# Kernel optimization log

Measured on AMD Instinct MI355X. Metric: run time of the kernel, lower is better.

Reference implementation:

```python
import jax, jax.numpy as jnp
import numpy as np

EPS = 1e-6

def rmsnorm(x, w):
    v = jnp.mean(x * x, axis=-1, keepdims=True)
    return x * jax.lax.rsqrt(v + EPS) * (1.0 + w)

def dense_glu(x, W, b):
    o = x @ W + b
    a, g = jnp.split(o, 2, axis=-1)
    return jax.nn.silu(a) * jax.nn.sigmoid(g)

def setup_inputs() -> dict:
    key = jax.random.key(0)
    ks = jax.random.split(key, 24)
    B, Nh, N, D, R = 2, 192, 256, 128, 20
    s_heavy = jax.random.normal(ks[0], (B, Nh, D), jnp.float32)
    v_all = jax.random.normal(ks[1], (B, N, 3, D), jnp.float32)
    rbf = jax.random.uniform(ks[2], (B, N, N, R), jnp.float32)
    dir_ij = jax.random.normal(ks[3], (B, N, N, 3), jnp.float32)
    mask_ij = jax.random.uniform(ks[4], (B, N, N), jnp.float32)
    is_hydrogen = jax.random.bernoulli(ks[5], 0.25, (B, N))
    p = lambda k, sh: 0.05 * jax.random.normal(k, sh, jnp.float32)
    return {
        "s_heavy": s_heavy, "v_all": v_all, "rbf": rbf, "dir_ij": dir_ij,
        "mask_ij": mask_ij, "is_hydrogen": is_hydrogen,
        "h_emb": jax.random.normal(ks[6], (D,), jnp.float32),
        "W_filter": p(ks[7], (R, 3 * D)), "b_filter": p(ks[8], (3 * D,)),
        "norm1_w": p(ks[9], (D,)),
        "W_i1": p(ks[10], (D, 2 * D)), "b_i1": p(ks[11], (2 * D,)),
        "W_i2": p(ks[12], (D, 3 * D)), "b_i2": p(ks[13], (3 * D,)),
        "norm2_w": p(ks[14], (D,)),
        "W_m1": p(ks[15], (2 * D, 2 * D)), "b_m1": p(ks[16], (2 * D,)),
        "W_m2": p(ks[17], (D, 3 * D)), "b_m2": p(ks[18], (3 * D,)),
        "W_mu": p(ks[19], (D, 2 * D)),
    }

def reference(s_heavy, v_all, rbf, dir_ij, mask_ij, is_hydrogen, h_emb,
              W_filter, b_filter, norm1_w, W_i1, b_i1, W_i2, b_i2,
              norm2_w, W_m1, b_m1, W_m2, b_m2, W_mu):
    B, N, _, D = v_all.shape
    Nh = s_heavy.shape[1]
    # hydrogen reinforcement: pad heavy-atom scalars to N_all, fill H slots with embedding
    s_pad = jnp.pad(s_heavy, ((0, 0), (0, N - Nh), (0, 0)))
    s_all = jnp.where(is_hydrogen[..., None], h_emb, s_pad)
    # --- interaction ---
    Wij = rbf @ W_filter + b_filter                                  # (B,N,N,3D)
    x = dense_glu(rmsnorm(s_all, norm1_w), W_i1, b_i1) @ W_i2 + b_i2  # (B,N,3D)
    x_inter = Wij * x[:, None, :, :] * mask_ij[..., None]            # (B,N,N,3D)
    dq, dmuR, dmumu = jnp.split(x_inter, 3, axis=-1)                 # each (B,N,N,D)
    q = s_all + dq.sum(axis=2)
    # dmu[b,i,r,d] = sum_j dmuR*dir + dmumu*mu_j (fused reductions over neighbor j)
    dmu = (jnp.einsum('bijd,bijr->bird', dmuR, dir_ij)
           + jnp.einsum('bijd,bjrd->bird', dmumu, v_all))            # (B,N,3,D)
    mu = v_all + dmu
    # --- mixing ---
    mu_mix = mu @ W_mu                                               # (B,N,3,2D)
    mu_V, mu_W = jnp.split(mu_mix, 2, axis=-1)
    mu_Vn = jnp.sqrt(jnp.sum(mu_V * mu_V, axis=2) + EPS)             # (B,N,D)
    ctx = jnp.concatenate([rmsnorm(q, norm2_w), mu_Vn], axis=-1)
    x2 = dense_glu(ctx, W_m1, b_m1) @ W_m2 + b_m2                    # (B,N,3D)
    dq_i, dmu_i, dqmu_i = jnp.split(x2, 3, axis=-1)
    q_out = q + dq_i + dqmu_i * jnp.sum(mu_V * mu_W, axis=2)
    mu_out = mu + dmu_i[:, :, None, :] * mu_W
    return q_out[:, :Nh, :], mu_out
```

## Files before the change

kernel.cpp:

```cpp
#include <hip/hip_runtime.h>
#include <hip/hip_bf16.h>

#define DEV static __device__ __forceinline__

typedef __attribute__((ext_vector_type(8))) short bf16x8;
typedef __attribute__((ext_vector_type(4))) float f32x4;

DEV float sigm(float x) { return 1.0f / (1.0f + __expf(-x)); }

DEV unsigned pack2bf(float a, float b) {
    unsigned r;
    asm("v_cvt_pk_bf16_f32 %0, %1, %2" : "=v"(r) : "v"(a), "v"(b));
    return r;
}
DEV unsigned short f2bf(float a) {
    unsigned ua = __float_as_uint(a);
    return (unsigned short)((ua + 0x7FFF + ((ua >> 16) & 1)) >> 16);
}
DEV float bfu2f(unsigned short u) { return __uint_as_float(((unsigned)u) << 16); }
DEV float lo2f(unsigned u) { return __uint_as_float(u << 16); }
DEV float hi2f(unsigned u) { return __uint_as_float(u & 0xffff0000u); }


__global__ __launch_bounds__(256) void kA(
    const float* __restrict__ s_heavy, const int* __restrict__ is_h,
    const float* __restrict__ h_emb, const float* __restrict__ norm1_w,
    const float* __restrict__ W_i1, const float* __restrict__ b_i1,
    const float* __restrict__ W_i2, const float* __restrict__ b_i2,
    const float* __restrict__ W_mu, const float* __restrict__ W_m1,
    const float* __restrict__ W_m2, const float* __restrict__ W_filter,
    const float* __restrict__ b_filter,
    float* __restrict__ s_all, float* __restrict__ x,
    unsigned* __restrict__ Wmu_p, unsigned* __restrict__ Wm1_p,
    unsigned* __restrict__ Wm2_p, unsigned* __restrict__ Wfb_p)
{
    const int blk = blockIdx.x;
    const int t = threadIdx.x;
    if (blk >= 512) {
        const int idx0 = (blk - 512) * 256 + t;
        {
            int k2 = idx0 >> 8, c = idx0 & 255;
            Wmu_p[(k2 >> 1) * 512 + c * 2 + (k2 & 1)] =
                pack2bf(W_mu[(2 * k2) * 256 + c], W_mu[(2 * k2 + 1) * 256 + c]);
        }
        #pragma unroll
        for (int r = 0; r < 2; ++r) {
            int s = idx0 + r * 16384;
            int k2 = s >> 8, c = s & 255;
            Wm1_p[(k2 >> 1) * 512 + c * 2 + (k2 & 1)] =
                pack2bf(W_m1[(2 * k2) * 256 + c], W_m1[(2 * k2 + 1) * 256 + c]);
        }
        for (int s = idx0; s < 24576; s += 16384) {
            int k2 = s / 384, c = s - k2 * 384;
            Wm2_p[(k2 >> 1) * 768 + c * 2 + (k2 & 1)] =
                pack2bf(W_m2[(2 * k2) * 384 + c], W_m2[(2 * k2 + 1) * 384 + c]);
        }
        for (int s = idx0; s < 4032; s += 16384) {
            int e = 2 * s;
            float v0 = (e < 7680) ? W_filter[e] : b_filter[e - 7680];
            float v1 = (e + 1 < 7680) ? W_filter[e + 1] : b_filter[e + 1 - 7680];
            Wfb_p[s] = pack2bf(v0, v1);
        }
        return;
    }
    const int bi = blk;
    const int b = bi >> 8, i = bi & 255;
    __shared__ float y[128];
    __shared__ float o[256];
    __shared__ float h[128];
    __shared__ float red[4];

    float s = 0.f;
    if (t < 128) {
        if (is_h[bi] != 0) s = h_emb[t];
        else if (i < 192) s = s_heavy[(b * 192 + i) * 128 + t];
        s_all[bi * 128 + t] = s;
    }
    float ss = s * s;
    #pragma unroll
    for (int off = 32; off > 0; off >>= 1) ss += __shfl_xor(ss, off, 64);
    if ((t & 63) == 0) red[t >> 6] = ss;
    __syncthreads();
    float v = (red[0] + red[1] + red[2] + red[3]) * (1.0f / 128.0f);
    float inv = rsqrtf(v + 1e-6f);
    if (t < 128) y[t] = s * inv * (1.0f + norm1_w[t]);
    __syncthreads();

    {
        float acc0 = 0.f, acc1 = 0.f;
        #pragma unroll 8
        for (int k = 0; k < 128; k += 2) {
            acc0 += y[k] * W_i1[k * 256 + t];
            acc1 += y[k + 1] * W_i1[(k + 1) * 256 + t];
        }
        o[t] = acc0 + acc1 + b_i1[t];
    }
    __syncthreads();
    if (t < 128) {
        float a = o[t], g = o[t + 128];
        h[t] = a * sigm(a) * sigm(g);
    }
    __syncthreads();
    for (int c = t; c < 384; c += 256) {
        float a0 = b_i2[c], a1 = 0.f;
        #pragma unroll 8
        for (int k = 0; k < 128; k += 2) {
            a0 += h[k] * W_i2[k * 384 + c];
            a1 += h[k + 1] * W_i2[(k + 1) * 384 + c];
        }
        x[(long)bi * 384 + c] = a0 + a1;
    }
}

__global__ __launch_bounds__(640) void kX2(
    const float* __restrict__ x, const float* __restrict__ v_all,
    unsigned* __restrict__ Bg)
{
    int blk = blockIdx.x;
    const int g = blk & 3; blk >>= 2;
    const int kt = blk & 7; const int b = blk >> 3;
    const int col = threadIdx.x;
    const int j0 = kt * 32 + g * 8;
    const float* xb = x + (long)b * 98304;
    const float* vb = v_all + (long)b * 98304;

    float vals[8];
    if (col < 256) {
        #pragma unroll
        for (int jj = 0; jj < 8; ++jj) vals[jj] = xb[(j0 + jj) * 384 + col];
    } else {
        const int cg = col - 256, r3 = cg >> 7, c3 = cg & 127;
        #pragma unroll
        for (int jj = 0; jj < 8; ++jj) {
            const int j = j0 + jj;
            vals[jj] = vb[j * 384 + r3 * 128 + c3] * xb[j * 384 + 256 + c3];
        }
    }
    uint4 outv = make_uint4(pack2bf(vals[0], vals[1]), pack2bf(vals[2], vals[3]),
                            pack2bf(vals[4], vals[5]), pack2bf(vals[6], vals[7]));
    *(uint4*)&Bg[(((long)(b * 8 + kt) * 4 + g) * 640 + col) * 4] = outv;
}

__global__ __launch_bounds__(512, 4) void kBC(
    const float* __restrict__ rbf, const float* __restrict__ dir_ij,
    const float* __restrict__ mask_ij, const float* __restrict__ v_all,
    const float* __restrict__ s_all, const unsigned* __restrict__ Bg,
    const unsigned* __restrict__ Wmu_p, const float* __restrict__ norm2_w,
    const unsigned* __restrict__ Wm1_p, const float* __restrict__ b_m1,
    const unsigned* __restrict__ Wm2_p, const float* __restrict__ b_m2,
    const unsigned* __restrict__ Wfb_p,
    float* __restrict__ q_out, float* __restrict__ mu_out)
{
    const int bi = blockIdx.x, b = bi >> 8, i = bi & 255;
    const int t = threadIdx.x;
    const int lane = t & 63, w = t >> 6, g = lane >> 4, l16 = lane & 15;

    __shared__ __align__(16) unsigned short A16[96 * 264];
    __shared__ unsigned short dir16[768];
    __shared__ float m_s[256];

    if (t < 256) m_s[t] = mask_ij[(long)bi * 256 + t];
    for (int idx = t; idx < 768; idx += 512) dir16[idx] = f2bf(dir_ij[(long)bi * 768 + idx]);
    {
        unsigned* Az = (unsigned*)A16;
        for (int s2 = t; s2 < 1452; s2 += 512) Az[2772 + s2] = 0;
        if (t < 132) Az[12540 + t] = 0;
    }
    __syncthreads();

    {
        unsigned* A32 = (unsigned*)A16;
        #pragma unroll
        for (int it = 0; it < 5; ++it) {
            const int idx = it * 512 + t;
            const int j2 = idx / 20, r = idx - j2 * 20;
            const int j = 2 * j2;
            const float v0 = rbf[(long)bi * 5120 + j2 * 40 + r];
            const float v1 = rbf[(long)bi * 5120 + j2 * 40 + 20 + r];
            const float vm0 = v0 * m_s[j], vm1 = v1 * m_s[j + 1];
            const float d00 = bfu2f(dir16[j * 3 + 0]), d01 = bfu2f(dir16[j * 3 + 3]);
            const float d10 = bfu2f(dir16[j * 3 + 1]), d11 = bfu2f(dir16[j * 3 + 4]);
            const float d20 = bfu2f(dir16[j * 3 + 2]), d21 = bfu2f(dir16[j * 3 + 5]);
            A32[r * 132 + j2]        = pack2bf(vm0, vm1);
            A32[(32 + r) * 132 + j2] = pack2bf(vm0 * d00, vm1 * d01);
            A32[(53 + r) * 132 + j2] = pack2bf(vm0 * d10, vm1 * d11);
            A32[(74 + r) * 132 + j2] = pack2bf(vm0 * d20, vm1 * d21);
        }
        if (t < 128) {
            const int j2 = t, j = 2 * t;
            const float m0 = m_s[j], m1 = m_s[j + 1];
            const float d00 = bfu2f(dir16[j * 3 + 0]), d01 = bfu2f(dir16[j * 3 + 3]);
            const float d10 = bfu2f(dir16[j * 3 + 1]), d11 = bfu2f(dir16[j * 3 + 4]);
            const float d20 = bfu2f(dir16[j * 3 + 2]), d21 = bfu2f(dir16[j * 3 + 5]);
            A32[20 * 132 + j2] = pack2bf(m0, m1);
            A32[52 * 132 + j2] = pack2bf(m0 * d00, m1 * d01);
            A32[73 * 132 + j2] = pack2bf(m0 * d10, m1 * d11);
            A32[94 * 132 + j2] = pack2bf(m0 * d20, m1 * d21);
        }
    }
    __syncthreads();

    int colR[4];
    #pragma unroll
    for (int ci = 0; ci < 4; ++ci) {
        int ct = (w < 2) ? (4 * w + ci) : (4 * w + 8 + ci);
        colR[ci] = ct * 16 + l16;
    }
    const int col2 = (8 + w) * 16 + l16;

    const unsigned* BgB = Bg + (long)b * 81920;
    const unsigned short* Wfb16 = (const unsigned short*)Wfb_p;

    f32x4 accR[4][2];
    f32x4 acc2[4];
    #pragma unroll
    for (int ci = 0; ci < 4; ++ci) {
        #pragma unroll
        for (int rt = 0; rt < 2; ++rt) accR[ci][rt] = {0.f, 0.f, 0.f, 0.f};
        acc2[ci] = {0.f, 0.f, 0.f, 0.f};
    }

    #pragma unroll 2
    for (int kt = 0; kt < 8; ++kt) {
        bf16x8 af[6];
        #pragma unroll
        for (int rt = 0; rt < 6; ++rt)
            af[rt] = *(const bf16x8*)&A16[(rt * 16 + l16) * 264 + kt * 32 + g * 8];
        const unsigned* Bk = BgB + ((long)kt * 4 + g) * 640 * 4;
        bf16x8 bfr[5];
        #pragma unroll
        for (int u = 0; u < 4; ++u)
            bfr[u] = *(const bf16x8*)&Bk[colR[u] * 4];
        bfr[4] = *(const bf16x8*)&Bk[col2 * 4];
        #pragma unroll
        for (int ci = 0; ci < 4; ++ci) {
            accR[ci][0] = __builtin_amdgcn_mfma_f32_16x16x32_bf16(af[0], bfr[ci], accR[ci][0], 0, 0, 0);
            accR[ci][1] = __builtin_amdgcn_mfma_f32_16x16x32_bf16(af[1], bfr[ci], accR[ci][1], 0, 0, 0);
        }
        #pragma unroll
        for (int rt = 0; rt < 4; ++rt)
            acc2[rt] = __builtin_amdgcn_mfma_f32_16x16x32_bf16(af[2 + rt], bfr[4], acc2[rt], 0, 0, 0);
    }

    float p3[3] = {0.f, 0.f, 0.f};
    {
        const int c = 128 + 16 * w + l16;
        #pragma unroll
        for (int rt = 0; rt < 4; ++rt) {
            #pragma unroll
            for (int e = 0; e < 4; ++e) {
                int l = rt * 16 + g * 4 + e;
                if (l < 63) {
                    int r3 = (l >= 42) ? 2 : ((l >= 21) ? 1 : 0);
                    int rr = l - 21 * r3;
                    float wgt = bfu2f((rr < 20) ? Wfb16[rr * 384 + c] : Wfb16[7680 + c]);
                    p3[r3] += wgt * acc2[rt][e];
                }
            }
        }
        #pragma unroll
        for (int r3 = 0; r3 < 3; ++r3) {
            p3[r3] += __shfl_xor(p3[r3], 16, 64);
            p3[r3] += __shfl_xor(p3[r3], 32, 64);
        }
    }
    float pq[4];
    #pragma unroll
    for (int ci = 0; ci < 4; ++ci) {
        const int cwf = (w < 2) ? colR[ci] : (256 + ((colR[ci] - 256) & 127));
        float p = 0.f;
        #pragma unroll
        for (int rt = 0; rt < 2; ++rt) {
            #pragma unroll
            for (int e = 0; e < 4; ++e) {
                int row = rt * 16 + g * 4 + e;
                if (row <= 20) {
                    float wgt = bfu2f((row < 20) ? Wfb16[row * 384 + cwf] : Wfb16[7680 + cwf]);
                    p += wgt * accR[ci][rt][e];
                }
            }
        }
        p += __shfl_xor(p, 16, 64);
        p += __shfl_xor(p, 32, 64);
        pq[ci] = p;
    }
    const float vpre = (t < 384) ? v_all[(long)bi * 384 + t] : 0.f;
    __syncthreads();

    float* fb      = (float*)A16;
    float* dmuR_s  = fb;
    float* dmumu_s = fb + 384;
    float* q_s     = fb + 768;
    float* mu_s    = fb + 896;
    float* part    = fb + 1280;
    float* muV     = fb + 2816;
    float* muW     = fb + 3200;
    float* ctx     = fb + 3584;
    float* o_part  = fb + 3840;
    float* hsm     = fb + 4352;
    float* x2s     = fb + 4480;
    float* red     = fb + 4864;

    if (lane < 16) {
        #pragma unroll
        for (int r3 = 0; r3 < 3; ++r3) dmuR_s[r3 * 128 + 16 * w + l16] = p3[r3];
        #pragma unroll
        for (int ci = 0; ci < 4; ++ci) {
            if (w < 2) {
                q_s[colR[ci]] = s_all[bi * 128 + colR[ci]] + pq[ci];
            } else {
                dmumu_s[colR[ci] - 256] = pq[ci];
            }
        }
    }
    __syncthreads();
    if (t < 384) mu_s[t] = vpre + dmuR_s[t] + dmumu_s[t];
    __syncthreads();

    const int c = t & 255, kh = t >> 8;
    float qv = (t < 128) ? q_s[t] : 0.f;

    {
        float m0 = 0.f, m1 = 0.f, m2 = 0.f;
        const int k40 = kh * 16;
        #pragma unroll 4
        for (int k4 = k40; k4 < k40 + 16; ++k4) {
            uint2 u = *(const uint2*)&Wmu_p[k4 * 512 + c * 2];
            const int k = 4 * k4;
            float w0 = lo2f(u.x), w1 = hi2f(u.x), w2 = lo2f(u.y), w3 = hi2f(u.y);
            m0 += mu_s[k] * w0 + mu_s[k + 1] * w1 + mu_s[k + 2] * w2 + mu_s[k + 3] * w3;
            m1 += mu_s[128 + k] * w0 + mu_s[128 + k + 1] * w1
                + mu_s[128 + k + 2] * w2 + mu_s[128 + k + 3] * w3;
            m2 += mu_s[256 + k] * w0 + mu_s[256 + k + 1] * w1
                + mu_s[256 + k + 2] * w2 + mu_s[256 + k + 3] * w3;
        }
        part[kh * 768 + c] = m0; part[kh * 768 + 256 + c] = m1; part[kh * 768 + 512 + c] = m2;
    }
    float ss = qv * qv;
    #pragma unroll
    for (int off = 32; off > 0; off >>= 1) ss += __shfl_xor(ss, off, 64);
    if ((t & 63) == 0) red[t >> 6] = ss;
    __syncthreads();
    for (int idx = t; idx < 768; idx += 512) {
        const int r3 = idx >> 8, cc = idx & 255;
        float val = part[idx] + part[768 + idx];
        if (cc < 128) muV[r3 * 128 + cc] = val;
        else          muW[r3 * 128 + (cc - 128)] = val;
    }
    __syncthreads();
    float mean = (red[0] + red[1] + red[2] + red[3] + red[4] + red[5] + red[6] + red[7])
                 * (1.0f / 128.0f);
    if (t < 128) {
        ctx[t] = qv * rsqrtf(mean + 1e-6f) * (1.0f + norm2_w[t]);
    } else if (t < 256) {
        int d2 = t - 128;
        ctx[t] = sqrtf(muV[d2] * muV[d2] + muV[128 + d2] * muV[128 + d2]
                       + muV[256 + d2] * muV[256 + d2] + 1e-6f);
    }
    __syncthreads();

    {
        float acc0 = 0.f, acc1 = 0.f;
        const int k40 = kh * 32;
        #pragma unroll 8
        for (int k4 = k40; k4 < k40 + 32; ++k4) {
            uint2 u = *(const uint2*)&Wm1_p[k4 * 512 + c * 2];
            const int k = 4 * k4;
            acc0 += ctx[k] * lo2f(u.x) + ctx[k + 1] * hi2f(u.x);
            acc1 += ctx[k + 2] * lo2f(u.y) + ctx[k + 3] * hi2f(u.y);
        }
        o_part[kh * 256 + c] = acc0 + acc1;
    }
    __syncthreads();
    if (t < 128) {
        float a  = o_part[t]       + o_part[256 + t]       + b_m1[t];
        float gg = o_part[t + 128] + o_part[256 + t + 128] + b_m1[t + 128];
        hsm[t] = a * sigm(a) * sigm(gg);
    }
    __syncthreads();
    if (t < 384) {
        float a0 = b_m2[t], a1 = 0.f;
        #pragma unroll 8
        for (int k4 = 0; k4 < 32; ++k4) {
            uint2 u = *(const uint2*)&Wm2_p[k4 * 768 + t * 2];
            const int k = 4 * k4;
            a0 += hsm[k] * lo2f(u.x) + hsm[k + 1] * hi2f(u.x);
            a1 += hsm[k + 2] * lo2f(u.y) + hsm[k + 3] * hi2f(u.y);
        }
        x2s[t] = a0 + a1;
    }
    __syncthreads();

    if (t < 128) {
        const int d = t;
        float vw = muV[d] * muW[d] + muV[128 + d] * muW[128 + d] + muV[256 + d] * muW[256 + d];
        if (i < 192)
            q_out[((long)b * 192 + i) * 128 + d] = qv + x2s[d] + x2s[256 + d] * vw;
        #pragma unroll
        for (int r = 0; r < 3; ++r)
            mu_out[((long)bi * 3 + r) * 128 + d] =
                mu_s[r * 128 + d] + x2s[128 + d] * muW[r * 128 + d];
    }
}

extern "C" void kernel_launch(void* const* d_in, const int* in_sizes, int n_in,
                              void* d_out, int out_size, void* d_ws, size_t ws_size,
                              hipStream_t stream) {
    (void)in_sizes; (void)n_in; (void)out_size;
    const float* s_heavy  = (const float*)d_in[0];
    const float* v_all    = (const float*)d_in[1];
    const float* rbf      = (const float*)d_in[2];
    const float* dir_ij   = (const float*)d_in[3];
    const float* mask_ij  = (const float*)d_in[4];
    const int*   is_h     = (const int*)d_in[5];
    const float* h_emb    = (const float*)d_in[6];
    const float* W_filter = (const float*)d_in[7];
    const float* b_filter = (const float*)d_in[8];
    const float* norm1_w  = (const float*)d_in[9];
    const float* W_i1     = (const float*)d_in[10];
    const float* b_i1     = (const float*)d_in[11];
    const float* W_i2     = (const float*)d_in[12];
    const float* b_i2     = (const float*)d_in[13];
    const float* norm2_w  = (const float*)d_in[14];
    const float* W_m1     = (const float*)d_in[15];
    const float* b_m1     = (const float*)d_in[16];
    const float* W_m2     = (const float*)d_in[17];
    const float* b_m2     = (const float*)d_in[18];
    const float* W_mu     = (const float*)d_in[19];

    const size_t need = (size_t)503744 * 4;
    if (ws_size < need) return;
    float* ws    = (float*)d_ws;
    float* s_all = ws;
    float* x     = ws + 65536;
    unsigned* Bg    = (unsigned*)(ws + 262144);
    unsigned* Wmu_p = (unsigned*)(ws + 425984);
    unsigned* Wm1_p = (unsigned*)(ws + 442368);
    unsigned* Wm2_p = (unsigned*)(ws + 475136);
    unsigned* Wfb_p = (unsigned*)(ws + 499712);

    float* q_out  = (float*)d_out;
    float* mu_out = q_out + 2 * 192 * 128;

    kA<<<576, 256, 0, stream>>>(s_heavy, is_h, h_emb, norm1_w, W_i1, b_i1, W_i2, b_i2,
                                W_mu, W_m1, W_m2, W_filter, b_filter,
                                s_all, x, Wmu_p, Wm1_p, Wm2_p, Wfb_p);
    kX2<<<64, 640, 0, stream>>>(x, v_all, Bg);
    kBC<<<512, 512, 0, stream>>>(rbf, dir_ij, mask_ij, v_all, s_all, Bg,
                                 Wmu_p, norm2_w, Wm1_p, b_m1, Wm2_p, b_m2, Wfb_p,
                                 q_out, mu_out);
}
```

Measured before the change: 46.71 us.

## Fuse bf16 B-operand packing into kA and vectorize shared-memory reads in kBC

Removes the separate kX2 launch by having each row block in kA write its x row and the v_all*x product directly into the packed bf16 Bg layout as scattered 16-bit stores. This cuts a kernel launch and the re-read of x from global memory, at the cost of uncoalesced short writes, and rounding now goes through a software f2bf instead of the hardware pack instruction. Separately, the small matvec loops in kBC now read their shared-memory operands as float4 vectors instead of scalars.

Measured after the change: 44.61 us. -4.5%, faster.

```diff
diff --git a/kernel.cpp b/kernel.cpp
--- a/kernel.cpp
+++ b/kernel.cpp
@@ -29,8 +29,9 @@
     const float* __restrict__ W_i2, const float* __restrict__ b_i2,
     const float* __restrict__ W_mu, const float* __restrict__ W_m1,
     const float* __restrict__ W_m2, const float* __restrict__ W_filter,
-    const float* __restrict__ b_filter,
+    const float* __restrict__ b_filter, const float* __restrict__ v_all,
     float* __restrict__ s_all, float* __restrict__ x,
+    unsigned short* __restrict__ Bg16,
     unsigned* __restrict__ Wmu_p, unsigned* __restrict__ Wm1_p,
     unsigned* __restrict__ Wm2_p, unsigned* __restrict__ Wfb_p)
 {
@@ -68,6 +69,7 @@
     __shared__ float y[128];
     __shared__ float o[256];
     __shared__ float h[128];
+    __shared__ float xrow[384];
     __shared__ float red[4];
 
     float s = 0.f;
@@ -108,37 +110,26 @@
             a0 += h[k] * W_i2[k * 384 + c];
             a1 += h[k + 1] * W_i2[(k + 1) * 384 + c];
         }
-        x[(long)bi * 384 + c] = a0 + a1;
-    }
-}
-
-__global__ __launch_bounds__(640) void kX2(
-    const float* __restrict__ x, const float* __restrict__ v_all,
-    unsigned* __restrict__ Bg)
-{
-    int blk = blockIdx.x;
-    const int g = blk & 3; blk >>= 2;
-    const int kt = blk & 7; const int b = blk >> 3;
-    const int col = threadIdx.x;
-    const int j0 = kt * 32 + g * 8;
-    const float* xb = x + (long)b * 98304;
-    const float* vb = v_all + (long)b * 98304;
-
-    float vals[8];
-    if (col < 256) {
-        #pragma unroll
-        for (int jj = 0; jj < 8; ++jj) vals[jj] = xb[(j0 + jj) * 384 + col];
-    } else {
-        const int cg = col - 256, r3 = cg >> 7, c3 = cg & 127;
-        #pragma unroll
-        for (int jj = 0; jj < 8; ++jj) {
-            const int j = j0 + jj;
-            vals[jj] = vb[j * 384 + r3 * 128 + c3] * xb[j * 384 + 256 + c3];
-        }
-    }
-    uint4 outv = make_uint4(pack2bf(vals[0], vals[1]), pack2bf(vals[2], vals[3]),
-                            pack2bf(vals[4], vals[5]), pack2bf(vals[6], vals[7]));
-    *(uint4*)&Bg[(((long)(b * 8 + kt) * 4 + g) * 640 + col) * 4] = outv;
+        float xv = a0 + a1;
+        x[(long)bi * 384 + c] = xv;
+        xrow[c] = xv;
+    }
+    __syncthreads();
+
+    {
+        const int j = i;
+        const int kt = j >> 5, g2 = (j >> 3) & 3, jj = j & 7;
+        const long base16 = (((long)(b * 8 + kt) * 4 + g2) * 640) * 8 + jj;
+        for (int col = t; col < 640; col += 256) {
+            float val;
+            if (col < 256) val = xrow[col];
+            else {
+                const int cg = col - 256;
+                val = v_all[(long)bi * 384 + cg] * xrow[256 + (cg & 127)];
+            }
+            Bg16[base16 + col * 8] = f2bf(val);
+        }
+    }
 }
 
 __global__ __launch_bounds__(512, 4) void kBC(
@@ -327,12 +318,13 @@
         for (int k4 = k40; k4 < k40 + 16; ++k4) {
             uint2 u = *(const uint2*)&Wmu_p[k4 * 512 + c * 2];
             const int k = 4 * k4;
+            float4 a0 = *(const float4*)&mu_s[k];
+            float4 a1 = *(const float4*)&mu_s[128 + k];
+            float4 a2 = *(const float4*)&mu_s[256 + k];
             float w0 = lo2f(u.x), w1 = hi2f(u.x), w2 = lo2f(u.y), w3 = hi2f(u.y);
-            m0 += mu_s[k] * w0 + mu_s[k + 1] * w1 + mu_s[k + 2] * w2 + mu_s[k + 3] * w3;
-            m1 += mu_s[128 + k] * w0 + mu_s[128 + k + 1] * w1
-                + mu_s[128 + k + 2] * w2 + mu_s[128 + k + 3] * w3;
-            m2 += mu_s[256 + k] * w0 + mu_s[256 + k + 1] * w1
-                + mu_s[256 + k + 2] * w2 + mu_s[256 + k + 3] * w3;
+            m0 += a0.x * w0 + a0.y * w1 + a0.z * w2 + a0.w * w3;
+            m1 += a1.x * w0 + a1.y * w1 + a1.z * w2 + a1.w * w3;
+            m2 += a2.x * w0 + a2.y * w1 + a2.z * w2 + a2.w * w3;
         }
         part[kh * 768 + c] = m0; part[kh * 768 + 256 + c] = m1; part[kh * 768 + 512 + c] = m2;
     }
@@ -365,9 +357,9 @@
         #pragma unroll 8
         for (int k4 = k40; k4 < k40 + 32; ++k4) {
             uint2 u = *(const uint2*)&Wm1_p[k4 * 512 + c * 2];
-            const int k = 4 * k4;
-            acc0 += ctx[k] * lo2f(u.x) + ctx[k + 1] * hi2f(u.x);
-            acc1 += ctx[k + 2] * lo2f(u.y) + ctx[k + 3] * hi2f(u.y);
+            float4 cx = *(const float4*)&ctx[4 * k4];
+            acc0 += cx.x * lo2f(u.x) + cx.y * hi2f(u.x);
+            acc1 += cx.z * lo2f(u.y) + cx.w * hi2f(u.y);
         }
         o_part[kh * 256 + c] = acc0 + acc1;
     }
@@ -383,9 +375,9 @@
         #pragma unroll 8
         for (int k4 = 0; k4 < 32; ++k4) {
             uint2 u = *(const uint2*)&Wm2_p[k4 * 768 + t * 2];
-            const int k = 4 * k4;
-            a0 += hsm[k] * lo2f(u.x) + hsm[k + 1] * hi2f(u.x);
-            a1 += hsm[k + 2] * lo2f(u.y) + hsm[k + 3] * hi2f(u.y);
+            float4 hx = *(const float4*)&hsm[4 * k4];
+            a0 += hx.x * lo2f(u.x) + hx.y * hi2f(u.x);
+            a1 += hx.z * lo2f(u.y) + hx.w * hi2f(u.y);
         }
         x2s[t] = a0 + a1;
     }
@@ -443,9 +435,9 @@
     float* mu_out = q_out + 2 * 192 * 128;
 
     kA<<<576, 256, 0, stream>>>(s_heavy, is_h, h_emb, norm1_w, W_i1, b_i1, W_i2, b_i2,
-                                W_mu, W_m1, W_m2, W_filter, b_filter,
-                                s_all, x, Wmu_p, Wm1_p, Wm2_p, Wfb_p);
-    kX2<<<64, 640, 0, stream>>>(x, v_all, Bg);
+                                W_mu, W_m1, W_m2, W_filter, b_filter, v_all,
+                                s_all, x, (unsigned short*)Bg,
+                                Wmu_p, Wm1_p, Wm2_p, Wfb_p);
     kBC<<<512, 512, 0, stream>>>(rbf, dir_ij, mask_ij, v_all, s_all, Bg,
                                  Wmu_p, norm2_w, Wm1_p, b_m1, Wm2_p, b_m2, Wfb_p,
                                  q_out, mu_out);
```
